# Optimization experiments

Hardware: AMD Instinct MI355X
Metric: run time of the kernel (lower is better)

## Reference

```python
import jax, jax.numpy as jnp
import numpy as np

C = 256  # input_channels == output_channels (residual add requires it)
EPS = 1e-5


def conv1d(x, w, b):
    # x: [B, Cin, L], w: [Cout, Cin, K], 'same' padding for K=3,p=1
    y = jax.lax.conv_general_dilated(x, w, window_strides=(1,), padding=[(1, 1)],
                                     dimension_numbers=('NCH', 'OIH', 'NCH'))
    return y + b[None, :, None]


def batchnorm(x, gamma, beta):
    # training-mode BN over (batch, length) per channel, biased variance
    m = jnp.mean(x, axis=(0, 2), keepdims=True)
    v = jnp.var(x, axis=(0, 2), keepdims=True)
    return (x - m) * jax.lax.rsqrt(v + EPS) * gamma[None, :, None] + beta[None, :, None]


def cross_attn(q_in, kv_in, res, qw, qb, kw, kb, vw, vb, ow, ob, g, be):
    q = conv1d(q_in, qw, qb)   # [B, C, L]
    k = conv1d(kv_in, kw, kb)  # [B, C, L]
    v = conv1d(kv_in, vw, vb)  # [B, C, L]
    scores = jnp.einsum('bcl,bcm->blm', q, k) / jnp.sqrt(jnp.float32(C))
    probs = jax.nn.softmax(scores, axis=-1)          # [B, L, L]
    ctx = jnp.einsum('blm,bcm->bcl', probs, v)       # [B, C, L]
    return batchnorm(conv1d(ctx, ow, ob), g, be) + res


def setup_inputs() -> dict:
    key = jax.random.key(0)
    ks = jax.random.split(key, 24)
    B, L = 16, 1024
    d = {
        'image': jax.random.normal(ks[0], (B, C, L), jnp.float32),
        'clinical': jax.random.normal(ks[1], (B, 1, L), jnp.float32),
    }
    def w(k, shape):
        return jax.random.normal(k, shape, jnp.float32) * 0.05
    # branch a: cli_to_img (query from image, key/value from clinical)
    d['a_qw'] = w(ks[2], (C, C, 3)); d['a_qb'] = w(ks[3], (C,))
    d['a_kw'] = w(ks[4], (C, 1, 3)); d['a_kb'] = w(ks[5], (C,))
    d['a_vw'] = w(ks[6], (C, 1, 3)); d['a_vb'] = w(ks[7], (C,))
    d['a_ow'] = w(ks[8], (C, C, 3)); d['a_ob'] = w(ks[9], (C,))
    d['a_g'] = jnp.ones((C,), jnp.float32); d['a_beta'] = jnp.zeros((C,), jnp.float32)
    # branch b: img_to_cli (query from clinical, key/value from image)
    d['b_qw'] = w(ks[10], (C, 1, 3)); d['b_qb'] = w(ks[11], (C,))
    d['b_kw'] = w(ks[12], (C, C, 3)); d['b_kb'] = w(ks[13], (C,))
    d['b_vw'] = w(ks[14], (C, C, 3)); d['b_vb'] = w(ks[15], (C,))
    d['b_ow'] = w(ks[16], (C, C, 3)); d['b_ob'] = w(ks[17], (C,))
    d['b_g'] = jnp.ones((C,), jnp.float32); d['b_beta'] = jnp.zeros((C,), jnp.float32)
    return d


def reference(image, clinical,
              a_qw, a_qb, a_kw, a_kb, a_vw, a_vb, a_ow, a_ob, a_g, a_beta,
              b_qw, b_qb, b_kw, b_kb, b_vw, b_vb, b_ow, b_ob, b_g, b_beta):
    cli_to_img = cross_attn(image, clinical, image,
                            a_qw, a_qb, a_kw, a_kb, a_vw, a_vb, a_ow, a_ob, a_g, a_beta)
    img_to_cli = cross_attn(clinical, image, image,
                            b_qw, b_qb, b_kw, b_kb, b_vw, b_vb, b_ow, b_ob, b_g, b_beta)
    return jnp.concatenate([cli_to_img, img_to_cli], axis=1)  # [B, 2C, L]
```

## Files before the change

### kernel.cpp

```cpp
#include <hip/hip_runtime.h>


typedef short bf16x8 __attribute__((ext_vector_type(8)));
typedef float f32x4 __attribute__((ext_vector_type(4)));

__device__ __forceinline__ unsigned short f2bf(float f) {
    union { float f; unsigned u; } v; v.f = f;
    unsigned r = v.u + 0x7fffu + ((v.u >> 16) & 1u);
    return (unsigned short)(r >> 16);
}
__device__ __forceinline__ float bf2f(unsigned short h) {
    union { unsigned u; float f; } v; v.u = ((unsigned)h) << 16;
    return v.f;
}

__device__ __forceinline__ void glds16(const void* g, void* l) {
    __builtin_amdgcn_global_load_lds(
        (const __attribute__((address_space(1))) unsigned int*)g,
        (__attribute__((address_space(3))) unsigned int*)l, 16, 0, 0);
}

#define TM 128
#define TN 128
#define BK 32

struct GOp {
    const unsigned short* A; const unsigned short* B; void* C;
    long sA, sB, sC;
    int lda, ldb, ldc, nxt, nyt, nz;
    const float* bias_row; const float* bias_col;
    float* stats; int stat_base;
};

__global__ __launch_bounds__(256)
void gemm_nt(GOp op0, GOp op1, int n0, int K, float alpha)
{
    __shared__ __attribute__((aligned(16))) char sh[34816];
    unsigned short* shs = (unsigned short*)sh;
    int id = blockIdx.x;
    const bool brn = (id >= n0);
    const GOp op = brn ? op1 : op0;
    if (brn) id -= n0;
    const int bz = id % op.nz;
    const int rem = id / op.nz;
    const int by = rem / op.nxt;
    const int bx = rem - by * op.nxt;

    const unsigned short* Ab = op.A + op.sA * bz;
    const unsigned short* Bb = op.B + op.sB * bz;
    const int lda = op.lda, ldb = op.ldb;
    const int i0 = by * TM;
    const int j0 = bx * TN;
    const int t = threadIdx.x;
    const int lane = t & 63;
    const int wave = t >> 6;
    const int wm = wave & 1, wn = wave >> 1;

    const int srow = wave * 16 + (lane >> 2);
    const int sc8 = (lane & 3) * 8;
    const unsigned short* gA0 = Ab + (long)(i0 + srow) * lda + sc8;
    const unsigned short* gA1 = gA0 + (long)64 * lda;
    const unsigned short* gB0 = Bb + (long)(j0 + srow) * ldb + sc8;
    const unsigned short* gB1 = gB0 + (long)64 * ldb;
    const int d0 = wave * 512;
    const int d1 = 2048 + wave * 512;

    f32x4 acc[4][4];
#pragma unroll
    for (int a_ = 0; a_ < 4; ++a_)
#pragma unroll
        for (int b_ = 0; b_ < 4; ++b_)
            acc[a_][b_] = (f32x4){0.f, 0.f, 0.f, 0.f};

    const int frow = lane & 15;
    const int fk = (lane >> 4) * 8;

    glds16(gA0, shs + d0);
    glds16(gA1, shs + d1);
    glds16(gB0, shs + 8192 + d0);
    glds16(gB1, shs + 8192 + d1);

    int cur = 0;
    for (int k0 = 0; k0 < K; k0 += BK) {
        __syncthreads();
        const int kn = k0 + BK;
        if (kn < K) {
            const int nb = cur ^ 1;
            glds16(gA0 + kn, shs + nb * 4096 + d0);
            glds16(gA1 + kn, shs + nb * 4096 + d1);
            glds16(gB0 + kn, shs + 8192 + nb * 4096 + d0);
            glds16(gB1 + kn, shs + 8192 + nb * 4096 + d1);
        }
        const unsigned short* la = shs + cur * 4096;
        const unsigned short* lb = shs + 8192 + cur * 4096;
        bf16x8 af[4], bfr[4];
#pragma unroll
        for (int mt = 0; mt < 4; ++mt)
            af[mt] = *(const bf16x8*)(&la[(wm * 64 + mt * 16 + frow) * BK + fk]);
#pragma unroll
        for (int nt = 0; nt < 4; ++nt)
            bfr[nt] = *(const bf16x8*)(&lb[(wn * 64 + nt * 16 + frow) * BK + fk]);
#pragma unroll
        for (int mt = 0; mt < 4; ++mt)
#pragma unroll
            for (int nt = 0; nt < 4; ++nt)
                acc[mt][nt] = __builtin_amdgcn_mfma_f32_16x16x32_bf16(af[mt], bfr[nt], acc[mt][nt], 0, 0, 0);
        cur ^= 1;
    }

    const int lr = (lane >> 4) * 4;
    const int lc = lane & 15;
    __syncthreads();

    unsigned short* tile = shs;
#pragma unroll
    for (int mt = 0; mt < 4; ++mt) {
#pragma unroll
        for (int nt = 0; nt < 4; ++nt) {
            const int col = wn * 64 + nt * 16 + lc;
            const float bc = op.bias_col ? op.bias_col[j0 + col] : 0.f;
#pragma unroll
            for (int r = 0; r < 4; ++r) {
                const int row = wm * 64 + mt * 16 + lr + r;
                const float brv = op.bias_row ? op.bias_row[i0 + row] : 0.f;
                tile[row * 136 + col] = f2bf(acc[mt][nt][r] * alpha + brv + bc);
            }
        }
    }
    __syncthreads();
    unsigned short* Cb = (unsigned short*)op.C + op.sC * bz;
#pragma unroll
    for (int p = 0; p < 8; ++p) {
        const int cid = p * 256 + t;
        const int row = cid >> 4;
        const int c8 = (cid & 15) * 8;
        const uint4 v = *(const uint4*)(tile + row * 136 + c8);
        *(uint4*)(Cb + (long)(i0 + row) * op.ldc + j0 + c8) = v;
    }
    if (op.stats) {
        const int row = t >> 1, half = t & 1;
        float s = 0.f, s2 = 0.f;
#pragma unroll
        for (int c = 0; c < 64; c += 8) {
            const bf16x8 v = *(const bf16x8*)(tile + row * 136 + half * 64 + c);
#pragma unroll
            for (int e = 0; e < 8; ++e) {
                const float f = bf2f((unsigned short)v[e]);
                s += f; s2 += f * f;
            }
        }
        s += __shfl_xor(s, 1);
        s2 += __shfl_xor(s2, 1);
        if (half == 0) {
            const int ch = op.stat_base + i0 + row;
            atomicAdd(&op.stats[ch], s);
            atomicAdd(&op.stats[512 + ch], s2);
        }
    }
}

__global__ __launch_bounds__(256)
void flash_attn(const unsigned short* __restrict__ QK,
                const unsigned short* __restrict__ qTb,
                const unsigned short* __restrict__ kTa,
                const unsigned short* __restrict__ va,
                const unsigned short* __restrict__ vb,
                unsigned short* __restrict__ ctxT)
{
    __shared__ __attribute__((aligned(16))) char sh[53248];
    unsigned short* Qs = (unsigned short*)sh;
    unsigned short* Ps = (unsigned short*)(sh + 33792);
    float* lts = (float*)(sh + 51200);

    const long sQK = 1024L * 512, sQT = 1024L * 256, sV = 256L * 1024;
    const int bid = blockIdx.x;
    const int z = bid & 31;
    const int l0 = (bid >> 5) * 64;
    const bool bb = (z >= 16);
    const int zz = bb ? z - 16 : z;
    const unsigned short* Qg = bb ? (qTb + (long)zz * sQT) : (QK + (long)zz * sQK);
    const int ldq = bb ? 256 : 512;
    const unsigned short* Kg = bb ? (QK + (long)zz * sQK + 256) : (kTa + (long)zz * sQT);
    const int ldk = bb ? 512 : 256;
    const unsigned short* Vg = (bb ? vb : va) + (long)zz * sV;
    unsigned short* Og = ctxT + ((long)z * 1026 + 1 + l0) * 256;
    const unsigned short* Qb = Qg + (long)l0 * ldq;

    const int t = threadIdx.x;
    const int lane = t & 63, w = t >> 6;
    const int g = lane >> 4, li = lane & 15;

#pragma unroll
    for (int p = 0; p < 8; ++p) {
        const int cid = p * 256 + t, row = cid >> 5, c8 = (cid & 31) * 8;
        const uint4 v = *(const uint4*)(Qb + (long)row * ldq + c8);
        *(uint4*)(Qs + row * 264 + c8) = v;
    }
    __syncthreads();

    f32x4 acc_o[4][4];
    f32x4 l_run[4];
#pragma unroll
    for (int mt = 0; mt < 4; ++mt) {
        l_run[mt] = (f32x4){0.f, 0.f, 0.f, 0.f};
#pragma unroll
        for (int nt = 0; nt < 4; ++nt)
            acc_o[mt][nt] = (f32x4){0.f, 0.f, 0.f, 0.f};
    }

    for (int m0 = 0; m0 < 1024; m0 += 128) {
        f32x4 acc_s[4][2];
#pragma unroll
        for (int mt = 0; mt < 4; ++mt) {
            acc_s[mt][0] = (f32x4){0.f, 0.f, 0.f, 0.f};
            acc_s[mt][1] = (f32x4){0.f, 0.f, 0.f, 0.f};
        }
        const unsigned short* Kt = Kg + (long)(m0 + w * 32) * ldk;
#pragma unroll
        for (int kt = 0; kt < 8; ++kt) {
            const bf16x8 bk0 = *(const bf16x8*)(Kt + (long)li * ldk + kt * 32 + g * 8);
            const bf16x8 bk1 = *(const bf16x8*)(Kt + (long)(16 + li) * ldk + kt * 32 + g * 8);
#pragma unroll
            for (int mt = 0; mt < 4; ++mt) {
                const bf16x8 aq = *(const bf16x8*)(Qs + (mt * 16 + li) * 264 + kt * 32 + g * 8);
                acc_s[mt][0] = __builtin_amdgcn_mfma_f32_16x16x32_bf16(aq, bk0, acc_s[mt][0], 0, 0, 0);
                acc_s[mt][1] = __builtin_amdgcn_mfma_f32_16x16x32_bf16(aq, bk1, acc_s[mt][1], 0, 0, 0);
            }
        }
        f32x4 rs[4];
#pragma unroll
        for (int mt = 0; mt < 4; ++mt) {
            rs[mt] = (f32x4){0.f, 0.f, 0.f, 0.f};
#pragma unroll
            for (int nt = 0; nt < 2; ++nt)
#pragma unroll
                for (int r = 0; r < 4; ++r) {
                    const float pv = __expf(acc_s[mt][nt][r] * 0.0625f);
                    acc_s[mt][nt][r] = pv;
                    rs[mt][r] += pv;
                }
        }
#pragma unroll
        for (int mask = 1; mask <= 8; mask <<= 1)
#pragma unroll
            for (int mt = 0; mt < 4; ++mt)
#pragma unroll
                for (int r = 0; r < 4; ++r)
                    rs[mt][r] += __shfl_xor(rs[mt][r], mask);
#pragma unroll
        for (int mt = 0; mt < 4; ++mt)
#pragma unroll
            for (int nt = 0; nt < 2; ++nt)
#pragma unroll
                for (int r = 0; r < 4; ++r)
                    Ps[(mt * 16 + g * 4 + r) * 136 + w * 32 + nt * 16 + li] =
                        f2bf(acc_s[mt][nt][r]);
        if (li == 0)
#pragma unroll
            for (int mt = 0; mt < 4; ++mt)
                *(f32x4*)(lts + w * 64 + mt * 16 + g * 4) = rs[mt];
        __syncthreads();
#pragma unroll
        for (int mt = 0; mt < 4; ++mt) {
            const int off = mt * 16 + g * 4;
            const f32x4 s0 = *(const f32x4*)(lts + off);
            const f32x4 s1 = *(const f32x4*)(lts + 64 + off);
            const f32x4 s2 = *(const f32x4*)(lts + 128 + off);
            const f32x4 s3 = *(const f32x4*)(lts + 192 + off);
            l_run[mt] += s0 + s1 + s2 + s3;
        }
#pragma unroll
        for (int kt2 = 0; kt2 < 4; ++kt2) {
            bf16x8 bv[4];
#pragma unroll
            for (int nt2 = 0; nt2 < 4; ++nt2)
                bv[nt2] = *(const bf16x8*)(Vg + (long)(w * 64 + nt2 * 16 + li) * 1024
                                           + m0 + kt2 * 32 + g * 8);
#pragma unroll
            for (int mt = 0; mt < 4; ++mt) {
                const bf16x8 ap = *(const bf16x8*)(Ps + (mt * 16 + li) * 136 + kt2 * 32 + g * 8);
#pragma unroll
                for (int nt2 = 0; nt2 < 4; ++nt2)
                    acc_o[mt][nt2] = __builtin_amdgcn_mfma_f32_16x16x32_bf16(ap, bv[nt2], acc_o[mt][nt2], 0, 0, 0);
            }
        }
        __syncthreads();
    }

    f32x4 inv[4];
#pragma unroll
    for (int mt = 0; mt < 4; ++mt)
#pragma unroll
        for (int r = 0; r < 4; ++r)
            inv[mt][r] = 1.f / l_run[mt][r];
#pragma unroll
    for (int mt = 0; mt < 4; ++mt)
#pragma unroll
        for (int nt2 = 0; nt2 < 4; ++nt2)
#pragma unroll
            for (int r = 0; r < 4; ++r)
                Qs[(mt * 16 + g * 4 + r) * 264 + w * 64 + nt2 * 16 + li] =
                    f2bf(acc_o[mt][nt2][r] * inv[mt][r]);
    __syncthreads();
#pragma unroll
    for (int p = 0; p < 8; ++p) {
        const int cid = p * 256 + t, row = cid >> 5, c8 = (cid & 31) * 8;
        *(uint4*)(Og + (long)row * 256 + c8) = *(const uint4*)(Qs + row * 264 + c8);
    }
}

__global__ __launch_bounds__(256)
void prep(const float* __restrict__ image, const float* __restrict__ cli,
          const float* __restrict__ a_qw, const float* __restrict__ a_qb,
          const float* __restrict__ a_kw, const float* __restrict__ a_kb,
          const float* __restrict__ a_vw, const float* __restrict__ a_vb,
          const float* __restrict__ a_ow,
          const float* __restrict__ b_qw, const float* __restrict__ b_qb,
          const float* __restrict__ b_kw, const float* __restrict__ b_kb,
          const float* __restrict__ b_vw, const float* __restrict__ b_vb,
          const float* __restrict__ b_ow,
          unsigned short* __restrict__ imgT, unsigned short* __restrict__ ctxT,
          unsigned short* __restrict__ kTa, unsigned short* __restrict__ va,
          unsigned short* __restrict__ qTb,
          unsigned short* __restrict__ W, float* __restrict__ qkb,
          float* __restrict__ sums)
{
    __shared__ char smem[64 * 65 * 4];
    const int b = blockIdx.x;
    const int t = threadIdx.x;
    if (b < 1024) {
        float* tile = (float*)smem;
        const int bt = b >> 6, rem = b & 63;
        const int l0 = (rem & 15) * 64, c0 = (rem >> 4) * 64;
        const float* xb = image + ((long)bt * 256 + c0) * 1024 + l0;
        for (int idx = t; idx < 4096; idx += 256) {
            const int cc = idx >> 6, ll = idx & 63;
            tile[cc * 65 + ll] = xb[(long)cc * 1024 + ll];
        }
        __syncthreads();
        unsigned short* op = imgT + ((long)bt * 1026 + l0 + 1) * 256 + c0;
        for (int idx = t; idx < 4096; idx += 256) {
            const int ll = idx >> 6, cc = idx & 63;
            op[(long)ll * 256 + cc] = f2bf(tile[cc * 65 + ll]);
        }
    } else if (b < 1536) {
        float* xs = (float*)smem;
        const int local = b - 1024;
        const int bz = local >> 5;
        const int l0 = (local & 31) * 32;
        if (t < 34) {
            const int l = l0 + t - 1;
            xs[t] = (l >= 0 && l < 1024) ? cli[(long)bz * 1024 + l] : 0.f;
        }
        __syncthreads();
        for (int i = t; i < 32 * 256; i += 256) {
            const int r = i >> 8, c = i & 255;
            const float x0 = xs[r], x1 = xs[r + 1], x2 = xs[r + 2];
            const float kv = a_kw[c * 3] * x0 + a_kw[c * 3 + 1] * x1 + a_kw[c * 3 + 2] * x2 + a_kb[c];
            const float qv = b_qw[c * 3] * x0 + b_qw[c * 3 + 1] * x1 + b_qw[c * 3 + 2] * x2 + b_qb[c];
            const long base = ((long)bz * 1024 + l0 + r) * 256 + c;
            kTa[base] = f2bf(kv);
            qTb[base] = f2bf(qv);
        }
        for (int i = t; i < 32 * 256; i += 256) {
            const int c = i >> 5, r = i & 31;
            const float x0 = xs[r], x1 = xs[r + 1], x2 = xs[r + 2];
            const float vv = a_vw[c * 3] * x0 + a_vw[c * 3 + 1] * x1 + a_vw[c * 3 + 2] * x2 + a_vb[c];
            va[((long)bz * 256 + c) * 1024 + l0 + r] = f2bf(vv);
        }
    } else if (b < 5376) {
        const int i = (b - 1536) * 256 + t;
        const int row = i / 768;
        const int kk = i - row * 768;
        const int j = kk >> 8, ci = kk & 255;
        const float* src = (row < 256) ? a_qw : (row < 512) ? b_kw
                         : (row < 768) ? b_vw : (row < 1024) ? a_ow : b_ow;
        const int r = row & 255;
        W[i] = f2bf(src[r * 768 + ci * 3 + j]);
    } else {
        const int i = (b - 5376) * 256 + t;
        if (i < 512) {
            qkb[i] = (i < 256) ? a_qb[i] : b_kb[i - 256];
        } else if (i < 512 + 8192) {
            const int p = i - 512;
            const int bi = p >> 9, rr = (p >> 8) & 1, c = p & 255;
            imgT[((long)bi * 1026 + (rr ? 1025 : 0)) * 256 + c] = 0;
        } else if (i < 512 + 8192 + 16384) {
            const int p = i - 512 - 8192;
            const int bz = p >> 9, rr = (p >> 8) & 1, c = p & 255;
            ctxT[((long)bz * 1026 + (rr ? 1025 : 0)) * 256 + c] = 0;
        } else if (i < 512 + 8192 + 16384 + 1024) {
            sums[i - 512 - 8192 - 16384] = 0.f;
        }
    }
}

__global__ __launch_bounds__(256)
void bn_finalize(const float* __restrict__ sums,
                 const float* __restrict__ ag, const float* __restrict__ abeta,
                 const float* __restrict__ bg, const float* __restrict__ bbeta,
                 float* __restrict__ ss)
{
    const int ch = blockIdx.x * 256 + threadIdx.x;
    const int branch = ch >> 8, c = ch & 255;
    const float mean = sums[ch] * (1.f / 16384.f);
    const float var = sums[512 + ch] * (1.f / 16384.f) - mean * mean;
    const float inv = rsqrtf(var + 1e-5f);
    const float g = branch ? bg[c] : ag[c];
    const float be = branch ? bbeta[c] : abeta[c];
    const float sc = g * inv;
    ss[ch] = sc;
    ss[512 + ch] = be - mean * sc;
}

__global__ __launch_bounds__(256)
void bn_apply(const unsigned short* __restrict__ Y, const float* __restrict__ img,
              const float* __restrict__ ss, float* __restrict__ out)
{
    const long i4 = (long)blockIdx.x * 256 + threadIdx.x;
    const long e = i4 * 4;
    const int l = (int)(e & 1023);
    const int ch = (int)((e >> 10) & 511);
    const int b = (int)(e >> 19);
    const int branch = ch >> 8, c = ch & 255;
    const float sc = ss[ch], sh = ss[512 + ch];
    const long yoff = (((long)(branch * 16 + b)) * 256 + c) * 1024 + l;
    const long ioff = ((long)b * 256 + c) * 1024 + l;
    const ushort4 yv = *(const ushort4*)(Y + yoff);
    const float4 iv = *(const float4*)(img + ioff);
    float4 o;
    o.x = bf2f(yv.x) * sc + sh + iv.x;
    o.y = bf2f(yv.y) * sc + sh + iv.y;
    o.z = bf2f(yv.z) * sc + sh + iv.z;
    o.w = bf2f(yv.w) * sc + sh + iv.w;
    *(float4*)(out + e) = o;
}

extern "C" void kernel_launch(void* const* d_in, const int* in_sizes, int n_in,
                              void* d_out, int out_size, void* d_ws, size_t ws_size,
                              hipStream_t stream)
{
    const float* image    = (const float*)d_in[0];
    const float* clinical = (const float*)d_in[1];
    const float* a_qw = (const float*)d_in[2];  const float* a_qb = (const float*)d_in[3];
    const float* a_kw = (const float*)d_in[4];  const float* a_kb = (const float*)d_in[5];
    const float* a_vw = (const float*)d_in[6];  const float* a_vb = (const float*)d_in[7];
    const float* a_ow = (const float*)d_in[8];  const float* a_ob = (const float*)d_in[9];
    const float* a_g  = (const float*)d_in[10]; const float* a_be = (const float*)d_in[11];
    const float* b_qw = (const float*)d_in[12]; const float* b_qb = (const float*)d_in[13];
    const float* b_kw = (const float*)d_in[14]; const float* b_kb = (const float*)d_in[15];
    const float* b_vw = (const float*)d_in[16]; const float* b_vb = (const float*)d_in[17];
    const float* b_ow = (const float*)d_in[18]; const float* b_ob = (const float*)d_in[19];
    const float* b_g  = (const float*)d_in[20]; const float* b_be = (const float*)d_in[21];
    float* out = (float*)d_out;

    char* ws = (char*)d_ws;
    const long MB = 1048576L;
    unsigned short* imgT = (unsigned short*)(ws);
    unsigned short* ctxT = (unsigned short*)(ws + 9 * MB);
    unsigned short* kTa  = (unsigned short*)(ws + 27 * MB);
    unsigned short* qTb  = (unsigned short*)(ws + 36 * MB);
    unsigned short* va   = (unsigned short*)(ws + 46 * MB);
    unsigned short* vb   = (unsigned short*)(ws + 54 * MB);
    unsigned short* QK   = (unsigned short*)(ws + 62 * MB);
    unsigned short* Y    = (unsigned short*)(ws + 142 * MB);
    unsigned short* W    = (unsigned short*)(ws + 174 * MB);
    float*          qkb  = (float*)(ws + 176 * MB);
    float*          ss   = qkb + 512;
    float*          sums = qkb + 1536;
    unsigned short* Wqk = W;
    unsigned short* Wvb = W + 512L * 768;
    unsigned short* Woa = W + 768L * 768;
    unsigned short* Wob = W + 1024L * 768;

    const dim3 blk(256);
    const long sIT = 1026L * 256, sQK = 1024L * 512, sV = 256L * 1024;

    prep<<<5478, blk, 0, stream>>>(image, clinical,
                                   a_qw, a_qb, a_kw, a_kb, a_vw, a_vb, a_ow,
                                   b_qw, b_qb, b_kw, b_kb, b_vw, b_vb, b_ow,
                                   imgT, ctxT, kTa, va, qTb, W, qkb, sums);
    {
        GOp opQ = {imgT, Wqk, QK, sIT, 0, sQK, 256, 768, 512, 4, 8, 16, nullptr, qkb, nullptr, 0};
        GOp opV = {Wvb, imgT, vb, 0, sIT, sV, 768, 256, 1024, 8, 2, 16, b_vb, nullptr, nullptr, 0};
        gemm_nt<<<768, blk, 0, stream>>>(opQ, opV, 512, 768, 1.f);
    }
    flash_attn<<<512, blk, 0, stream>>>(QK, qTb, kTa, va, vb, ctxT);
    {
        GOp opA = {Woa, ctxT, Y, 0, sIT, sV, 768, 256, 1024, 8, 2, 16, a_ob, nullptr, sums, 0};
        GOp opB = {Wob, ctxT + 16 * sIT, Y + 16 * sV, 0, sIT, sV, 768, 256, 1024, 8, 2, 16, b_ob, nullptr, sums, 256};
        gemm_nt<<<512, blk, 0, stream>>>(opA, opB, 256, 768, 1.f);
    }
    bn_finalize<<<2, blk, 0, stream>>>(sums, a_g, a_be, b_g, b_be, ss);
    bn_apply<<<8192, blk, 0, stream>>>(Y, image, ss, out);
}
```

Measured before the change: 265.7 us.

## Split flash attention work across eight waves per block instead of four

The flash_attn kernel now launches 512-thread blocks. Each of the eight waves computes scores for 16 keys instead of 32 and accumulates 32 output channels instead of 64. The per-wave row-sum partials are now reduced across eight slots in shared memory, which exactly fills the remaining LDS space. The aim is more resident waves per CU to hide global K/V load latency, and fewer registers per thread for accumulators. The cost is more sharing of the Q/P shared-memory reads across waves and more cross-wave reduction work.

```diff
diff --git a/kernel.cpp b/kernel.cpp
--- a/kernel.cpp
+++ b/kernel.cpp
@@ -159,7 +159,7 @@
     }
 }
 
-__global__ __launch_bounds__(256)
+__global__ __launch_bounds__(512, 4)
 void flash_attn(const unsigned short* __restrict__ QK,
                 const unsigned short* __restrict__ qTb,
                 const unsigned short* __restrict__ kTa,
@@ -191,40 +191,36 @@
     const int g = lane >> 4, li = lane & 15;
 
 #pragma unroll
-    for (int p = 0; p < 8; ++p) {
-        const int cid = p * 256 + t, row = cid >> 5, c8 = (cid & 31) * 8;
+    for (int p = 0; p < 4; ++p) {
+        const int cid = p * 512 + t, row = cid >> 5, c8 = (cid & 31) * 8;
         const uint4 v = *(const uint4*)(Qb + (long)row * ldq + c8);
         *(uint4*)(Qs + row * 264 + c8) = v;
     }
     __syncthreads();
 
-    f32x4 acc_o[4][4];
+    f32x4 acc_o[4][2];
     f32x4 l_run[4];
 #pragma unroll
     for (int mt = 0; mt < 4; ++mt) {
         l_run[mt] = (f32x4){0.f, 0.f, 0.f, 0.f};
 #pragma unroll
-        for (int nt = 0; nt < 4; ++nt)
+        for (int nt = 0; nt < 2; ++nt)
             acc_o[mt][nt] = (f32x4){0.f, 0.f, 0.f, 0.f};
     }
 
     for (int m0 = 0; m0 < 1024; m0 += 128) {
-        f32x4 acc_s[4][2];
-#pragma unroll
-        for (int mt = 0; mt < 4; ++mt) {
-            acc_s[mt][0] = (f32x4){0.f, 0.f, 0.f, 0.f};
-            acc_s[mt][1] = (f32x4){0.f, 0.f, 0.f, 0.f};
-        }
-        const unsigned short* Kt = Kg + (long)(m0 + w * 32) * ldk;
+        f32x4 acc_s[4];
+#pragma unroll
+        for (int mt = 0; mt < 4; ++mt)
+            acc_s[mt] = (f32x4){0.f, 0.f, 0.f, 0.f};
+        const unsigned short* Kt = Kg + (long)(m0 + w * 16) * ldk;
 #pragma unroll
         for (int kt = 0; kt < 8; ++kt) {
-            const bf16x8 bk0 = *(const bf16x8*)(Kt + (long)li * ldk + kt * 32 + g * 8);
-            const bf16x8 bk1 = *(const bf16x8*)(Kt + (long)(16 + li) * ldk + kt * 32 + g * 8);
+            const bf16x8 bk = *(const bf16x8*)(Kt + (long)li * ldk + kt * 32 + g * 8);
 #pragma unroll
             for (int mt = 0; mt < 4; ++mt) {
                 const bf16x8 aq = *(const bf16x8*)(Qs + (mt * 16 + li) * 264 + kt * 32 + g * 8);
-                acc_s[mt][0] = __builtin_amdgcn_mfma_f32_16x16x32_bf16(aq, bk0, acc_s[mt][0], 0, 0, 0);
-                acc_s[mt][1] = __builtin_amdgcn_mfma_f32_16x16x32_bf16(aq, bk1, acc_s[mt][1], 0, 0, 0);
+                acc_s[mt] = __builtin_amdgcn_mfma_f32_16x16x32_bf16(aq, bk, acc_s[mt], 0, 0, 0);
             }
         }
         f32x4 rs[4];
@@ -232,13 +228,11 @@
         for (int mt = 0; mt < 4; ++mt) {
             rs[mt] = (f32x4){0.f, 0.f, 0.f, 0.f};
 #pragma unroll
-            for (int nt = 0; nt < 2; ++nt)
-#pragma unroll
-                for (int r = 0; r < 4; ++r) {
-                    const float pv = __expf(acc_s[mt][nt][r] * 0.0625f);
-                    acc_s[mt][nt][r] = pv;
-                    rs[mt][r] += pv;
-                }
+            for (int r = 0; r < 4; ++r) {
+                const float pv = __expf(acc_s[mt][r] * 0.0625f);
+                acc_s[mt][r] = pv;
+                rs[mt][r] += pv;
+            }
         }
 #pragma unroll
         for (int mask = 1; mask <= 8; mask <<= 1)
@@ -250,11 +244,8 @@
 #pragma unroll
         for (int mt = 0; mt < 4; ++mt)
 #pragma unroll
-            for (int nt = 0; nt < 2; ++nt)
-#pragma unroll
-                for (int r = 0; r < 4; ++r)
-                    Ps[(mt * 16 + g * 4 + r) * 136 + w * 32 + nt * 16 + li] =
-                        f2bf(acc_s[mt][nt][r]);
+            for (int r = 0; r < 4; ++r)
+                Ps[(mt * 16 + g * 4 + r) * 136 + w * 16 + li] = f2bf(acc_s[mt][r]);
         if (li == 0)
 #pragma unroll
             for (int mt = 0; mt < 4; ++mt)
@@ -263,24 +254,24 @@
 #pragma unroll
         for (int mt = 0; mt < 4; ++mt) {
             const int off = mt * 16 + g * 4;
-            const f32x4 s0 = *(const f32x4*)(lts + off);
-            const f32x4 s1 = *(const f32x4*)(lts + 64 + off);
-            const f32x4 s2 = *(const f32x4*)(lts + 128 + off);
-            const f32x4 s3 = *(const f32x4*)(lts + 192 + off);
-            l_run[mt] += s0 + s1 + s2 + s3;
+            f32x4 s = *(const f32x4*)(lts + off);
+#pragma unroll
+            for (int w2 = 1; w2 < 8; ++w2)
+                s += *(const f32x4*)(lts + w2 * 64 + off);
+            l_run[mt] += s;
         }
 #pragma unroll
         for (int kt2 = 0; kt2 < 4; ++kt2) {
-            bf16x8 bv[4];
-#pragma unroll
-            for (int nt2 = 0; nt2 < 4; ++nt2)
-                bv[nt2] = *(const bf16x8*)(Vg + (long)(w * 64 + nt2 * 16 + li) * 1024
+            bf16x8 bv[2];
+#pragma unroll
+            for (int nt2 = 0; nt2 < 2; ++nt2)
+                bv[nt2] = *(const bf16x8*)(Vg + (long)(w * 32 + nt2 * 16 + li) * 1024
                                            + m0 + kt2 * 32 + g * 8);
 #pragma unroll
             for (int mt = 0; mt < 4; ++mt) {
                 const bf16x8 ap = *(const bf16x8*)(Ps + (mt * 16 + li) * 136 + kt2 * 32 + g * 8);
 #pragma unroll
-                for (int nt2 = 0; nt2 < 4; ++nt2)
+                for (int nt2 = 0; nt2 < 2; ++nt2)
                     acc_o[mt][nt2] = __builtin_amdgcn_mfma_f32_16x16x32_bf16(ap, bv[nt2], acc_o[mt][nt2], 0, 0, 0);
             }
         }
@@ -296,15 +287,15 @@
 #pragma unroll
     for (int mt = 0; mt < 4; ++mt)
 #pragma unroll
-        for (int nt2 = 0; nt2 < 4; ++nt2)
+        for (int nt2 = 0; nt2 < 2; ++nt2)
 #pragma unroll
             for (int r = 0; r < 4; ++r)
-                Qs[(mt * 16 + g * 4 + r) * 264 + w * 64 + nt2 * 16 + li] =
+                Qs[(mt * 16 + g * 4 + r) * 264 + w * 32 + nt2 * 16 + li] =
                     f2bf(acc_o[mt][nt2][r] * inv[mt][r]);
     __syncthreads();
 #pragma unroll
-    for (int p = 0; p < 8; ++p) {
-        const int cid = p * 256 + t, row = cid >> 5, c8 = (cid & 31) * 8;
+    for (int p = 0; p < 4; ++p) {
+        const int cid = p * 512 + t, row = cid >> 5, c8 = (cid & 31) * 8;
         *(uint4*)(Og + (long)row * 256 + c8) = *(const uint4*)(Qs + row * 264 + c8);
     }
 }
@@ -474,6 +465,7 @@
     unsigned short* Wob = W + 1024L * 768;
 
     const dim3 blk(256);
+    const dim3 blk2(512);
     const long sIT = 1026L * 256, sQK = 1024L * 512, sV = 256L * 1024;
 
     prep<<<5478, blk, 0, stream>>>(image, clinical,
@@ -485,7 +477,7 @@
         GOp opV = {Wvb, imgT, vb, 0, sIT, sV, 768, 256, 1024, 8, 2, 16, b_vb, nullptr, nullptr, 0};
         gemm_nt<<<768, blk, 0, stream>>>(opQ, opV, 512, 768, 1.f);
     }
-    flash_attn<<<512, blk, 0, stream>>>(QK, qTb, kTa, va, vb, ctxT);
+    flash_attn<<<512, blk2, 0, stream>>>(QK, qTb, kTa, va, vb, ctxT);
     {
         GOp opA = {Woa, ctxT, Y, 0, sIT, sV, 768, 256, 1024, 8, 2, 16, a_ob, nullptr, sums, 0};
         GOp opB = {Wob, ctxT + 16 * sIT, Y + 16 * sV, 0, sIT, sV, 768, 256, 1024, 8, 2, 16, b_ob, nullptr, sums, 256};
```

New measurement: 278.6 us. 4.8% more time.

## Double-buffer P tile and overlap PV with next QK in flash attention

Applied to the files above, without the earlier changes.

The flash attention loop now double-buffers the probability tile in shared memory. The PV matmul for the previous key block is interleaved with the QK^T matmul for the current block, which removes one barrier per iteration. K fragments are prefetched into registers before the PV work to hide global latency. Row-sum reduction is deferred to after the loop instead of shuffling and exchanging through LDS each iteration, LDS row padding shrinks to 260/132, and launch bounds request two blocks per CU; together these raise register pressure and LDS size, and the new padding may change bank-conflict behaviour.

```diff
diff --git a/kernel.cpp b/kernel.cpp
--- a/kernel.cpp
+++ b/kernel.cpp
@@ -159,7 +159,7 @@
     }
 }
 
-__global__ __launch_bounds__(256)
+__global__ __launch_bounds__(256, 2)
 void flash_attn(const unsigned short* __restrict__ QK,
                 const unsigned short* __restrict__ qTb,
                 const unsigned short* __restrict__ kTa,
@@ -167,10 +167,11 @@
                 const unsigned short* __restrict__ vb,
                 unsigned short* __restrict__ ctxT)
 {
-    __shared__ __attribute__((aligned(16))) char sh[53248];
+    __shared__ __attribute__((aligned(16))) char sh[68096];
     unsigned short* Qs = (unsigned short*)sh;
-    unsigned short* Ps = (unsigned short*)(sh + 33792);
-    float* lts = (float*)(sh + 51200);
+    unsigned short* Ps0 = (unsigned short*)(sh + 33280);
+    unsigned short* Ps1 = (unsigned short*)(sh + 50176);
+    float* lts = (float*)(sh + 67072);
 
     const long sQK = 1024L * 512, sQT = 1024L * 256, sV = 256L * 1024;
     const int bid = blockIdx.x;
@@ -194,7 +195,7 @@
     for (int p = 0; p < 8; ++p) {
         const int cid = p * 256 + t, row = cid >> 5, c8 = (cid & 31) * 8;
         const uint4 v = *(const uint4*)(Qb + (long)row * ldq + c8);
-        *(uint4*)(Qs + row * 264 + c8) = v;
+        *(uint4*)(Qs + row * 260 + c8) = v;
     }
     __syncthreads();
 
@@ -208,104 +209,117 @@
             acc_o[mt][nt] = (f32x4){0.f, 0.f, 0.f, 0.f};
     }
 
+#define PV_TILE(mm0, psrc)                                                      \
+    {                                                                           \
+        _Pragma("unroll")                                                       \
+        for (int kt2 = 0; kt2 < 4; ++kt2) {                                     \
+            bf16x8 bv[4];                                                       \
+            _Pragma("unroll")                                                   \
+            for (int nt2 = 0; nt2 < 4; ++nt2)                                   \
+                bv[nt2] = *(const bf16x8*)(Vg + (long)(w * 64 + nt2 * 16 + li) * 1024 \
+                                           + (mm0) + kt2 * 32 + g * 8);         \
+            _Pragma("unroll")                                                   \
+            for (int mt = 0; mt < 4; ++mt) {                                    \
+                const bf16x8 ap = *(const bf16x8*)((psrc) + (mt * 16 + li) * 132 \
+                                                   + kt2 * 32 + g * 8);         \
+                _Pragma("unroll")                                               \
+                for (int nt2 = 0; nt2 < 4; ++nt2)                               \
+                    acc_o[mt][nt2] = __builtin_amdgcn_mfma_f32_16x16x32_bf16(   \
+                        ap, bv[nt2], acc_o[mt][nt2], 0, 0, 0);                  \
+            }                                                                   \
+        }                                                                       \
+    }
+
     for (int m0 = 0; m0 < 1024; m0 += 128) {
+        const int buf = (m0 >> 7) & 1;
+        unsigned short* Pw = buf ? Ps1 : Ps0;
+        const unsigned short* Kt = Kg + (long)(m0 + w * 32) * ldk;
+        bf16x8 kf[8][2];
+#pragma unroll
+        for (int kt = 0; kt < 8; ++kt) {
+            kf[kt][0] = *(const bf16x8*)(Kt + (long)li * ldk + kt * 32 + g * 8);
+            kf[kt][1] = *(const bf16x8*)(Kt + (long)(16 + li) * ldk + kt * 32 + g * 8);
+        }
+        if (m0) {
+            const unsigned short* Pr = buf ? Ps0 : Ps1;
+            PV_TILE(m0 - 128, Pr)
+        }
         f32x4 acc_s[4][2];
 #pragma unroll
         for (int mt = 0; mt < 4; ++mt) {
             acc_s[mt][0] = (f32x4){0.f, 0.f, 0.f, 0.f};
             acc_s[mt][1] = (f32x4){0.f, 0.f, 0.f, 0.f};
         }
-        const unsigned short* Kt = Kg + (long)(m0 + w * 32) * ldk;
 #pragma unroll
         for (int kt = 0; kt < 8; ++kt) {
-            const bf16x8 bk0 = *(const bf16x8*)(Kt + (long)li * ldk + kt * 32 + g * 8);
-            const bf16x8 bk1 = *(const bf16x8*)(Kt + (long)(16 + li) * ldk + kt * 32 + g * 8);
 #pragma unroll
             for (int mt = 0; mt < 4; ++mt) {
-                const bf16x8 aq = *(const bf16x8*)(Qs + (mt * 16 + li) * 264 + kt * 32 + g * 8);
-                acc_s[mt][0] = __builtin_amdgcn_mfma_f32_16x16x32_bf16(aq, bk0, acc_s[mt][0], 0, 0, 0);
-                acc_s[mt][1] = __builtin_amdgcn_mfma_f32_16x16x32_bf16(aq, bk1, acc_s[mt][1], 0, 0, 0);
+                const bf16x8 aq = *(const bf16x8*)(Qs + (mt * 16 + li) * 260 + kt * 32 + g * 8);
+                acc_s[mt][0] = __builtin_amdgcn_mfma_f32_16x16x32_bf16(aq, kf[kt][0], acc_s[mt][0], 0, 0, 0);
+                acc_s[mt][1] = __builtin_amdgcn_mfma_f32_16x16x32_bf16(aq, kf[kt][1], acc_s[mt][1], 0, 0, 0);
             }
         }
-        f32x4 rs[4];
-#pragma unroll
-        for (int mt = 0; mt < 4; ++mt) {
-            rs[mt] = (f32x4){0.f, 0.f, 0.f, 0.f};
+#pragma unroll
+        for (int mt = 0; mt < 4; ++mt)
 #pragma unroll
             for (int nt = 0; nt < 2; ++nt)
 #pragma unroll
                 for (int r = 0; r < 4; ++r) {
                     const float pv = __expf(acc_s[mt][nt][r] * 0.0625f);
                     acc_s[mt][nt][r] = pv;
-                    rs[mt][r] += pv;
+                    l_run[mt][r] += pv;
                 }
-        }
-#pragma unroll
-        for (int mask = 1; mask <= 8; mask <<= 1)
-#pragma unroll
-            for (int mt = 0; mt < 4; ++mt)
+#pragma unroll
+        for (int mt = 0; mt < 4; ++mt)
+#pragma unroll
+            for (int nt = 0; nt < 2; ++nt)
 #pragma unroll
                 for (int r = 0; r < 4; ++r)
-                    rs[mt][r] += __shfl_xor(rs[mt][r], mask);
+                    Pw[(mt * 16 + g * 4 + r) * 132 + w * 32 + nt * 16 + li] =
+                        f2bf(acc_s[mt][nt][r]);
+        __syncthreads();
+    }
+    PV_TILE(896, Ps1)
+#undef PV_TILE
+
+#pragma unroll
+    for (int mask = 1; mask <= 8; mask <<= 1)
 #pragma unroll
         for (int mt = 0; mt < 4; ++mt)
 #pragma unroll
-            for (int nt = 0; nt < 2; ++nt)
-#pragma unroll
-                for (int r = 0; r < 4; ++r)
-                    Ps[(mt * 16 + g * 4 + r) * 136 + w * 32 + nt * 16 + li] =
-                        f2bf(acc_s[mt][nt][r]);
-        if (li == 0)
-#pragma unroll
-            for (int mt = 0; mt < 4; ++mt)
-                *(f32x4*)(lts + w * 64 + mt * 16 + g * 4) = rs[mt];
-        __syncthreads();
-#pragma unroll
-        for (int mt = 0; mt < 4; ++mt) {
-            const int off = mt * 16 + g * 4;
-            const f32x4 s0 = *(const f32x4*)(lts + off);
-            const f32x4 s1 = *(const f32x4*)(lts + 64 + off);
-            const f32x4 s2 = *(const f32x4*)(lts + 128 + off);
-            const f32x4 s3 = *(const f32x4*)(lts + 192 + off);
-            l_run[mt] += s0 + s1 + s2 + s3;
-        }
-#pragma unroll
-        for (int kt2 = 0; kt2 < 4; ++kt2) {
-            bf16x8 bv[4];
-#pragma unroll
-            for (int nt2 = 0; nt2 < 4; ++nt2)
-                bv[nt2] = *(const bf16x8*)(Vg + (long)(w * 64 + nt2 * 16 + li) * 1024
-                                           + m0 + kt2 * 32 + g * 8);
-#pragma unroll
-            for (int mt = 0; mt < 4; ++mt) {
-                const bf16x8 ap = *(const bf16x8*)(Ps + (mt * 16 + li) * 136 + kt2 * 32 + g * 8);
-#pragma unroll
-                for (int nt2 = 0; nt2 < 4; ++nt2)
-                    acc_o[mt][nt2] = __builtin_amdgcn_mfma_f32_16x16x32_bf16(ap, bv[nt2], acc_o[mt][nt2], 0, 0, 0);
-            }
-        }
-        __syncthreads();
-    }
+            for (int r = 0; r < 4; ++r)
+                l_run[mt][r] += __shfl_xor(l_run[mt][r], mask);
+    if (li == 0)
+#pragma unroll
+        for (int mt = 0; mt < 4; ++mt)
+            *(f32x4*)(lts + w * 64 + mt * 16 + g * 4) = l_run[mt];
+    __syncthreads();
 
     f32x4 inv[4];
 #pragma unroll
+    for (int mt = 0; mt < 4; ++mt) {
+        const int off = mt * 16 + g * 4;
+        const f32x4 s0 = *(const f32x4*)(lts + off);
+        const f32x4 s1 = *(const f32x4*)(lts + 64 + off);
+        const f32x4 s2 = *(const f32x4*)(lts + 128 + off);
+        const f32x4 s3 = *(const f32x4*)(lts + 192 + off);
+#pragma unroll
+        for (int r = 0; r < 4; ++r)
+            inv[mt][r] = 1.f / (s0[r] + s1[r] + s2[r] + s3[r]);
+    }
+#pragma unroll
     for (int mt = 0; mt < 4; ++mt)
 #pragma unroll
-        for (int r = 0; r < 4; ++r)
-            inv[mt][r] = 1.f / l_run[mt][r];
-#pragma unroll
-    for (int mt = 0; mt < 4; ++mt)
-#pragma unroll
         for (int nt2 = 0; nt2 < 4; ++nt2)
 #pragma unroll
             for (int r = 0; r < 4; ++r)
-                Qs[(mt * 16 + g * 4 + r) * 264 + w * 64 + nt2 * 16 + li] =
+                Qs[(mt * 16 + g * 4 + r) * 260 + w * 64 + nt2 * 16 + li] =
                     f2bf(acc_o[mt][nt2][r] * inv[mt][r]);
     __syncthreads();
 #pragma unroll
     for (int p = 0; p < 8; ++p) {
         const int cid = p * 256 + t, row = cid >> 5, c8 = (cid & 31) * 8;
-        *(uint4*)(Og + (long)row * 256 + c8) = *(const uint4*)(Qs + row * 264 + c8);
+        *(uint4*)(Og + (long)row * 256 + c8) = *(const uint4*)(Qs + row * 260 + c8);
     }
 }
 
```

Result: slower. 288.2 us (+8.5%).
